# Kernel optimization log

Hardware: AMD Instinct MI355X
Metric: run time of the kernel (lower is better)

Reference implementation:

```python
import jax, jax.numpy as jnp
import numpy as np

B, N, FE, T, OUT = 32, 2048, 32, 12, 3


def setup_inputs() -> dict:
    key = jax.random.key(0)
    ks = jax.random.split(key, 7)
    return {
        "x": jax.random.normal(ks[0], (B, N, FE, T), dtype=jnp.float32),
        "w_ih": jax.random.normal(ks[1], (3, FE), dtype=jnp.float32) * 0.1,
        "w_hh": jax.random.normal(ks[2], (3, 1), dtype=jnp.float32) * 0.1,
        "b_ih": jax.random.normal(ks[3], (3,), dtype=jnp.float32) * 0.1,
        "b_hh": jax.random.normal(ks[4], (3,), dtype=jnp.float32) * 0.1,
        "lin_w": jax.random.normal(ks[5], (OUT, T), dtype=jnp.float32) * 0.1,
        "lin_b": jax.random.normal(ks[6], (OUT,), dtype=jnp.float32) * 0.1,
        "unused": 0,
    }


def reference(x, w_ih, w_hh, b_ih, b_hh, lin_w, lin_b, unused):
    b, n, fe, t = x.shape
    # [B,N,Fe,T] -> [M,T,Fe] with M = B*N
    xs = jnp.transpose(x.reshape(-1, fe, t), (0, 2, 1))
    # Precompute input-to-gate projections for all timesteps: [M,T,3] (r,z,n gates)
    gates_x = jnp.einsum("mtf,gf->mtg", xs, w_ih) + b_ih
    wh = w_hh[:, 0]  # [3] recurrent weights, hidden size is 1

    def step(h, gx):
        # h: [M], gx: [M,3]
        r = jax.nn.sigmoid(gx[:, 0] + wh[0] * h + b_hh[0])
        z = jax.nn.sigmoid(gx[:, 1] + wh[1] * h + b_hh[1])
        nn_ = jnp.tanh(gx[:, 2] + r * (wh[2] * h + b_hh[2]))
        h_new = (1.0 - z) * nn_ + z * h
        return h_new, h_new

    h0 = jnp.zeros(xs.shape[0], dtype=x.dtype)
    _, hs = jax.lax.scan(step, h0, jnp.swapaxes(gates_x, 0, 1))  # [T,M]
    h = jax.nn.relu(hs.T)  # [M,T] (squeeze of [M,T,1])
    out = h @ lin_w.T + lin_b  # [M,OUT]
    return out.reshape(b, n, -1)
```

## Files before the change

kernel.cpp:

```cpp
#include <hip/hip_runtime.h>

#define FE_ 32
#define T_  12
#define M_  (32 * 2048)

__global__ __launch_bounds__(256) void gru_seq_kernel(
    const float* __restrict__ x,
    const float* __restrict__ w_ih,
    const float* __restrict__ w_hh,
    const float* __restrict__ b_ih,
    const float* __restrict__ b_hh,
    const float* __restrict__ lin_w,
    const float* __restrict__ lin_b,
    float* __restrict__ out)
{
    const int m = blockIdx.x * blockDim.x + threadIdx.x;
    if (m >= M_) return;

    float acc0[T_], acc1[T_], acc2[T_];
    const float bi0 = b_ih[0], bi1 = b_ih[1], bi2 = b_ih[2];
#pragma unroll
    for (int t = 0; t < T_; ++t) { acc0[t] = bi0; acc1[t] = bi1; acc2[t] = bi2; }

    const float4* __restrict__ xrow =
        (const float4*)(x + (size_t)m * (FE_ * T_));

#pragma unroll 4
    for (int f = 0; f < FE_; ++f) {
        const float4 a = xrow[f * 3 + 0];
        const float4 b = xrow[f * 3 + 1];
        const float4 c = xrow[f * 3 + 2];
        const float xv[T_] = { a.x, a.y, a.z, a.w,
                               b.x, b.y, b.z, b.w,
                               c.x, c.y, c.z, c.w };
        const float w0 = w_ih[0 * FE_ + f];
        const float w1 = w_ih[1 * FE_ + f];
        const float w2 = w_ih[2 * FE_ + f];
#pragma unroll
        for (int t = 0; t < T_; ++t) {
            acc0[t] = fmaf(xv[t], w0, acc0[t]);
            acc1[t] = fmaf(xv[t], w1, acc1[t]);
            acc2[t] = fmaf(xv[t], w2, acc2[t]);
        }
    }

    const float wh0 = w_hh[0], wh1 = w_hh[1], wh2 = w_hh[2];
    const float bh0 = b_hh[0], bh1 = b_hh[1], bh2 = b_hh[2];
    float o0 = lin_b[0], o1 = lin_b[1], o2 = lin_b[2];

    float h = 0.0f;
#pragma unroll
    for (int t = 0; t < T_; ++t) {
        const float r = 1.0f / (1.0f + __expf(-(acc0[t] + wh0 * h + bh0)));
        const float z = 1.0f / (1.0f + __expf(-(acc1[t] + wh1 * h + bh1)));
        const float y = acc2[t] + r * (wh2 * h + bh2);
        const float n = 1.0f - 2.0f / (1.0f + __expf(2.0f * y));
        h = (1.0f - z) * n + z * h;
        const float ht = h > 0.0f ? h : 0.0f;
        o0 = fmaf(ht, lin_w[0 * T_ + t], o0);
        o1 = fmaf(ht, lin_w[1 * T_ + t], o1);
        o2 = fmaf(ht, lin_w[2 * T_ + t], o2);
    }

    float* __restrict__ po = out + (size_t)m * 3;
    po[0] = o0; po[1] = o1; po[2] = o2;
}

extern "C" void kernel_launch(void* const* d_in, const int* in_sizes, int n_in,
                              void* d_out, int out_size, void* d_ws, size_t ws_size,
                              hipStream_t stream) {
    (void)in_sizes; (void)n_in; (void)d_ws; (void)ws_size; (void)out_size;
    const float* x     = (const float*)d_in[0];
    const float* w_ih  = (const float*)d_in[1];
    const float* w_hh  = (const float*)d_in[2];
    const float* b_ih  = (const float*)d_in[3];
    const float* b_hh  = (const float*)d_in[4];
    const float* lin_w = (const float*)d_in[5];
    const float* lin_b = (const float*)d_in[6];
    float* out = (float*)d_out;

    const int block = 256;
    const int grid = (M_ + block - 1) / block;
    gru_seq_kernel<<<grid, block, 0, stream>>>(x, w_ih, w_hh, b_ih, b_hh,
                                               lin_w, lin_b, out);
}
```

Before: 166.6 us.

## Split input projection across timesteps per thread and run recurrence from LDS

Work is reassigned so each block handles 32 sequences with 384 threads, one per (sequence, timestep). Each thread computes its three gate projections over the 32 features, and the results are staged in padded shared memory. After a barrier, 32 threads run the serial GRU recurrence and the output linear layer. This targets the poorly coalesced per-thread 1.5KB row reads and the high register pressure of the old one-thread-per-sequence layout. The cost is that most threads sit idle during the recurrence phase, and every block now pays for a barrier.

```diff
diff --git a/kernel.cpp b/kernel.cpp
--- a/kernel.cpp
+++ b/kernel.cpp
@@ -3,8 +3,11 @@
 #define FE_ 32
 #define T_  12
 #define M_  (32 * 2048)
+#define SEQ_PER_BLOCK 32
+#define THREADS (SEQ_PER_BLOCK * T_)
+#define LDS_STRIDE 37
 
-__global__ __launch_bounds__(256) void gru_seq_kernel(
+__global__ __launch_bounds__(THREADS) void gru_fused_kernel(
     const float* __restrict__ x,
     const float* __restrict__ w_ih,
     const float* __restrict__ w_hh,
@@ -14,56 +17,47 @@
     const float* __restrict__ lin_b,
     float* __restrict__ out)
 {
-    const int m = blockIdx.x * blockDim.x + threadIdx.x;
-    if (m >= M_) return;
+    __shared__ float gbuf[SEQ_PER_BLOCK * LDS_STRIDE];
 
-    float acc0[T_], acc1[T_], acc2[T_];
-    const float bi0 = b_ih[0], bi1 = b_ih[1], bi2 = b_ih[2];
+    const int tid = threadIdx.x;
+    const int s   = tid / T_;
+    const int t   = tid - s * T_;
+    const int m0  = blockIdx.x * SEQ_PER_BLOCK;
+
+    const float* __restrict__ xp = x + (size_t)(m0 + s) * (FE_ * T_) + t;
+    float a0 = b_ih[0], a1 = b_ih[1], a2 = b_ih[2];
 #pragma unroll
-    for (int t = 0; t < T_; ++t) { acc0[t] = bi0; acc1[t] = bi1; acc2[t] = bi2; }
+    for (int f = 0; f < FE_; ++f) {
+        const float xv = xp[f * T_];
+        a0 = fmaf(xv, w_ih[0 * FE_ + f], a0);
+        a1 = fmaf(xv, w_ih[1 * FE_ + f], a1);
+        a2 = fmaf(xv, w_ih[2 * FE_ + f], a2);
+    }
+    float* g = &gbuf[s * LDS_STRIDE + t * 3];
+    g[0] = a0; g[1] = a1; g[2] = a2;
+    __syncthreads();
 
-    const float4* __restrict__ xrow =
-        (const float4*)(x + (size_t)m * (FE_ * T_));
-
-#pragma unroll 4
-    for (int f = 0; f < FE_; ++f) {
-        const float4 a = xrow[f * 3 + 0];
-        const float4 b = xrow[f * 3 + 1];
-        const float4 c = xrow[f * 3 + 2];
-        const float xv[T_] = { a.x, a.y, a.z, a.w,
-                               b.x, b.y, b.z, b.w,
-                               c.x, c.y, c.z, c.w };
-        const float w0 = w_ih[0 * FE_ + f];
-        const float w1 = w_ih[1 * FE_ + f];
-        const float w2 = w_ih[2 * FE_ + f];
+    if (tid < SEQ_PER_BLOCK) {
+        const float wh0 = w_hh[0], wh1 = w_hh[1], wh2 = w_hh[2];
+        const float bh0 = b_hh[0], bh1 = b_hh[1], bh2 = b_hh[2];
+        float o0 = lin_b[0], o1 = lin_b[1], o2 = lin_b[2];
+        const float* __restrict__ gg = &gbuf[tid * LDS_STRIDE];
+        float h = 0.0f;
 #pragma unroll
-        for (int t = 0; t < T_; ++t) {
-            acc0[t] = fmaf(xv[t], w0, acc0[t]);
-            acc1[t] = fmaf(xv[t], w1, acc1[t]);
-            acc2[t] = fmaf(xv[t], w2, acc2[t]);
+        for (int tt = 0; tt < T_; ++tt) {
+            const float r = 1.0f / (1.0f + __expf(-(gg[tt * 3 + 0] + wh0 * h + bh0)));
+            const float z = 1.0f / (1.0f + __expf(-(gg[tt * 3 + 1] + wh1 * h + bh1)));
+            const float y = gg[tt * 3 + 2] + r * (wh2 * h + bh2);
+            const float n = 1.0f - 2.0f / (1.0f + __expf(2.0f * y));
+            h = (1.0f - z) * n + z * h;
+            const float ht = h > 0.0f ? h : 0.0f;
+            o0 = fmaf(ht, lin_w[0 * T_ + tt], o0);
+            o1 = fmaf(ht, lin_w[1 * T_ + tt], o1);
+            o2 = fmaf(ht, lin_w[2 * T_ + tt], o2);
         }
+        float* __restrict__ po = out + (size_t)(m0 + tid) * 3;
+        po[0] = o0; po[1] = o1; po[2] = o2;
     }
-
-    const float wh0 = w_hh[0], wh1 = w_hh[1], wh2 = w_hh[2];
-    const float bh0 = b_hh[0], bh1 = b_hh[1], bh2 = b_hh[2];
-    float o0 = lin_b[0], o1 = lin_b[1], o2 = lin_b[2];
-
-    float h = 0.0f;
-#pragma unroll
-    for (int t = 0; t < T_; ++t) {
-        const float r = 1.0f / (1.0f + __expf(-(acc0[t] + wh0 * h + bh0)));
-        const float z = 1.0f / (1.0f + __expf(-(acc1[t] + wh1 * h + bh1)));
-        const float y = acc2[t] + r * (wh2 * h + bh2);
-        const float n = 1.0f - 2.0f / (1.0f + __expf(2.0f * y));
-        h = (1.0f - z) * n + z * h;
-        const float ht = h > 0.0f ? h : 0.0f;
-        o0 = fmaf(ht, lin_w[0 * T_ + t], o0);
-        o1 = fmaf(ht, lin_w[1 * T_ + t], o1);
-        o2 = fmaf(ht, lin_w[2 * T_ + t], o2);
-    }
-
-    float* __restrict__ po = out + (size_t)m * 3;
-    po[0] = o0; po[1] = o1; po[2] = o2;
 }
 
 extern "C" void kernel_launch(void* const* d_in, const int* in_sizes, int n_in,
@@ -79,8 +73,7 @@
     const float* lin_b = (const float*)d_in[6];
     float* out = (float*)d_out;
 
-    const int block = 256;
-    const int grid = (M_ + block - 1) / block;
-    gru_seq_kernel<<<grid, block, 0, stream>>>(x, w_ih, w_hh, b_ih, b_hh,
-                                               lin_w, lin_b, out);
+    const int grid = M_ / SEQ_PER_BLOCK;
+    gru_fused_kernel<<<grid, THREADS, 0, stream>>>(x, w_ih, w_hh, b_ih, b_hh,
+                                                   lin_w, lin_b, out);
 }
```

Result: faster. 159.1 us (-4.5%).
